# Kernel optimization log

Measured on AMD Instinct MI355X. Metric: run time of the kernel, lower is better.

Reference implementation:

```python
import jax, jax.numpy as jnp
import numpy as np


def setup_inputs() -> dict:
    key = jax.random.key(0)
    kq, kk, kv = jax.random.split(key, 3)
    B, H, N, D = 2, 16, 2048, 64
    q = jax.random.normal(kq, (B, H, N, D), dtype=jnp.float32)
    k = jax.random.normal(kk, (B, H, N, D), dtype=jnp.float32)
    v = jax.random.normal(kv, (B, H, N, D), dtype=jnp.float32)
    return {"q": q, "k": k, "v": v}


def reference(q, k, v):
    # RBF-kernel causal attention: logits = -relu(||q-k||^2) / sqrt(D)
    B, H, N, D = q.shape
    sm_scale = 1.0 / jnp.sqrt(jnp.asarray(D, dtype=q.dtype))
    q_sq = jnp.sum(q * q, axis=-1)              # [B,H,N]
    k_sq = jnp.sum(k * k, axis=-1)              # [B,H,N]
    qk = jnp.einsum("bhmd,bhnd->bhmn", q, k)    # [B,H,N,N]
    dist_sq = q_sq[..., :, None] + k_sq[..., None, :] - 2.0 * qk
    dist_sq = jnp.maximum(dist_sq, 0.0)         # relu on squared distance
    logits = -dist_sq * sm_scale
    # causal mask: query m attends to keys n <= m
    causal = jnp.tril(jnp.ones((N, N), dtype=bool))
    logits = jnp.where(causal, logits, -jnp.inf)
    p = jax.nn.softmax(logits, axis=-1)
    out = jnp.einsum("bhmn,bhnd->bhmd", p, v)
    return out
```

## Files before the change

### kernel.cpp

```cpp
#include <hip/hip_runtime.h>

#define NN 2048
#define DD 64
#define C1 0.36067376f
#define C1H 0.18033688f

typedef _Float16 h8 __attribute__((ext_vector_type(8)));
typedef _Float16 h4 __attribute__((ext_vector_type(4)));
typedef float f32x16 __attribute__((ext_vector_type(16)));

union H8U4 { h8 v; unsigned u[4]; };

__global__ __launch_bounds__(64) void prep(const float* __restrict__ k,
                                           const float* __restrict__ v,
                                           _Float16* __restrict__ Ks,
                                           _Float16* __restrict__ Vs,
                                           float* __restrict__ hk) {
    __shared__ _Float16 T[32][72];
    const int jj = blockIdx.x, bh = blockIdx.y, lane = threadIdx.x;
    const int ln = lane & 31, lh = lane >> 5;
    const size_t ibase = (size_t)bh * NN * DD + (size_t)jj * 32 * DD;

    {
        const float* kr = k + ibase + (size_t)ln * DD;
        float s = 0.f;
#pragma unroll
        for (int c = 0; c < 4; ++c) {
            float4 a = *(const float4*)&kr[16 * c + 8 * lh];
            float4 b = *(const float4*)&kr[16 * c + 8 * lh + 4];
            h8 o = {(_Float16)a.x, (_Float16)a.y, (_Float16)a.z, (_Float16)a.w,
                    (_Float16)b.x, (_Float16)b.y, (_Float16)b.z, (_Float16)b.w};
            *(h8*)&Ks[((size_t)bh * 16384 + jj * 256 + c * 64 + lh * 32 + ln) * 8] = o;
            s += a.x*a.x + a.y*a.y + a.z*a.z + a.w*a.w
               + b.x*b.x + b.y*b.y + b.z*b.z + b.w*b.w;
        }
        s += __shfl_xor(s, 32);
        if (lh == 0) hk[bh * NN + jj * 32 + ln] = s * C1H;
    }

#pragma unroll
    for (int t = 0; t < 8; ++t) {
        int f = lane + 64 * t;
        int row = f >> 4, c4 = (f & 15) * 4;
        float4 a = *(const float4*)&v[ibase + (size_t)row * DD + c4];
        h4 hv = {(_Float16)a.x, (_Float16)a.y, (_Float16)a.z, (_Float16)a.w};
        *(h4*)&T[row][c4] = hv;
    }
    __syncthreads();
#pragma unroll
    for (int oc = 0; oc < 4; ++oc) {
        int o = oc >> 1, c = oc & 1;
        h8 r;
#pragma unroll
        for (int jx = 0; jx < 8; ++jx) r[jx] = T[16 * c + 8 * lh + jx][32 * o + ln];
        *(h8*)&Vs[((size_t)bh * 16384 + jj * 256 + o * 128 + c * 64 + lh * 32 + ln) * 8] = r;
    }
}

__global__ __launch_bounds__(128, 2) void rbf_attn(
    const float* __restrict__ q, const _Float16* __restrict__ Ks,
    const _Float16* __restrict__ Vs, const float* __restrict__ hk,
    float* __restrict__ out)
{
    const int tid = threadIdx.x;
    const int bh = blockIdx.x;
    const int qb = 31 - blockIdx.y;
    const int wv = tid >> 6, lane = tid & 63;
    const int ln = lane & 31, lh = lane >> 5;
    const int jmax = 2 * qb + wv;
    const int qrow = qb * 64 + wv * 32 + ln;
    const size_t fbase = (size_t)bh * NN * DD;

    h8 qf[4];
    {
        const float* qr = q + fbase + (size_t)qrow * DD;
#pragma unroll
        for (int c = 0; c < 4; ++c) {
            float4 a = *(const float4*)&qr[16 * c + 8 * lh];
            float4 b = *(const float4*)&qr[16 * c + 8 * lh + 4];
            qf[c] = h8{(_Float16)a.x, (_Float16)a.y, (_Float16)a.z, (_Float16)a.w,
                       (_Float16)b.x, (_Float16)b.y, (_Float16)b.z, (_Float16)b.w};
        }
    }

    const _Float16* Ksb = Ks + (size_t)bh * 131072;
    const _Float16* Vsb = Vs + (size_t)bh * 131072;
    const float4* hk4 = (const float4*)(hk + bh * NN);
    const int klq = (lh * 32 + ln) * 8;

    f32x16 O0, O1;
#pragma unroll
    for (int r = 0; r < 16; ++r) { O0[r] = 0.f; O1[r] = 0.f; }
    float lsum = 0.f, mrun = -INFINITY;

    auto loadT = [&](int jj, h8 (&kf)[4], h8 (&vf)[4], float4 (&hr)[4]) {
        const _Float16* kp = Ksb + (size_t)jj * 2048 + klq;
        const _Float16* vp = Vsb + (size_t)jj * 2048 + klq;
#pragma unroll
        for (int c = 0; c < 4; ++c) kf[c] = *(const h8*)(kp + c * 512);
#pragma unroll
        for (int oc = 0; oc < 4; ++oc)
            vf[oc] = *(const h8*)(vp + (oc >> 1) * 1024 + (oc & 1) * 512);
#pragma unroll
        for (int g = 0; g < 4; ++g) hr[g] = hk4[jj * 8 + g * 2 + lh];
    };

    auto comp = [&](int jj, h8 (&kf)[4], h8 (&vf)[4], float4 (&hr)[4]) {
        f32x16 S;
#pragma unroll
        for (int r = 0; r < 16; ++r) S[r] = 0.f;
#pragma unroll
        for (int c = 0; c < 4; ++c)
            S = __builtin_amdgcn_mfma_f32_32x32x16_f16(kf[c], qf[c], S, 0, 0, 0);

        const bool diag = (jj == jmax);
        float x[16];
#pragma unroll
        for (int r = 0; r < 16; ++r) {
            const float* hf = (const float*)&hr[r >> 2];
            float xv = fmaf(S[r], C1, -hf[r & 3]);
            if (diag) {
                int keyloc = (r & 3) + 8 * (r >> 2) + 4 * lh;
                if (keyloc > ln) xv = -INFINITY;
            }
            x[r] = xv;
        }
        float mt = x[0];
#pragma unroll
        for (int r = 1; r < 16; ++r) mt = fmaxf(mt, x[r]);
        mt = fmaxf(mt, __shfl_xor(mt, 32));
        float mnew = fmaxf(mrun, mt);
        float alpha = __builtin_amdgcn_exp2f(mrun - mnew);
        mrun = mnew;
        float p[16], ps = 0.f;
#pragma unroll
        for (int r = 0; r < 16; ++r) {
            p[r] = __builtin_amdgcn_exp2f(x[r] - mnew);
            ps += p[r];
        }
        lsum = fmaf(lsum, alpha, ps);
#pragma unroll
        for (int r = 0; r < 16; ++r) { O0[r] *= alpha; O1[r] *= alpha; }

        unsigned pk[8];
#pragma unroll
        for (int hh = 0; hh < 8; ++hh) {
            auto pr = __builtin_amdgcn_cvt_pkrtz(p[2 * hh], p[2 * hh + 1]);
            unsigned pu; __builtin_memcpy(&pu, &pr, 4);
            pk[hh] = pu;
        }
#pragma unroll
        for (int s = 0; s < 2; ++s) {
            unsigned send0 = lh ? pk[4 * s + 0] : pk[4 * s + 2];
            unsigned send1 = lh ? pk[4 * s + 1] : pk[4 * s + 3];
            unsigned r0 = (unsigned)__shfl_xor((int)send0, 32);
            unsigned r1 = (unsigned)__shfl_xor((int)send1, 32);
            H8U4 pb;
            pb.u[0] = lh ? r0 : pk[4 * s + 0];
            pb.u[1] = lh ? r1 : pk[4 * s + 1];
            pb.u[2] = lh ? pk[4 * s + 2] : r0;
            pb.u[3] = lh ? pk[4 * s + 3] : r1;
            O0 = __builtin_amdgcn_mfma_f32_32x32x16_f16(vf[s], pb.v, O0, 0, 0, 0);
            O1 = __builtin_amdgcn_mfma_f32_32x32x16_f16(vf[2 + s], pb.v, O1, 0, 0, 0);
        }
    };

    h8 kfA[4], vfA[4]; float4 hrA[4];
    h8 kfB[4], vfB[4]; float4 hrB[4];
    loadT(0, kfA, vfA, hrA);
    int jj = 0;
    while (true) {
        if (jj < jmax) loadT(jj + 1, kfB, vfB, hrB);
        comp(jj, kfA, vfA, hrA);
        if (++jj > jmax) break;
        if (jj < jmax) loadT(jj + 1, kfA, vfA, hrA);
        comp(jj, kfB, vfB, hrB);
        if (++jj > jmax) break;
    }

    float lt = lsum + __shfl_xor(lsum, 32);
    float inv = 1.f / lt;
    size_t ro = fbase + (size_t)qrow * DD;
#pragma unroll
    for (int g = 0; g < 4; ++g) {
        float4 o0 = make_float4(O0[4 * g + 0] * inv, O0[4 * g + 1] * inv,
                                O0[4 * g + 2] * inv, O0[4 * g + 3] * inv);
        *(float4*)&out[ro + 8 * g + 4 * lh] = o0;
        float4 o1 = make_float4(O1[4 * g + 0] * inv, O1[4 * g + 1] * inv,
                                O1[4 * g + 2] * inv, O1[4 * g + 3] * inv);
        *(float4*)&out[ro + 32 + 8 * g + 4 * lh] = o1;
    }
}

extern "C" void kernel_launch(void* const* d_in, const int* in_sizes, int n_in,
                              void* d_out, int out_size, void* d_ws, size_t ws_size,
                              hipStream_t stream) {
    (void)in_sizes; (void)n_in; (void)out_size; (void)ws_size;
    const float* q = (const float*)d_in[0];
    const float* k = (const float*)d_in[1];
    const float* v = (const float*)d_in[2];
    float* out = (float*)d_out;

    float* hk = (float*)d_ws;
    _Float16* Ks = (_Float16*)((char*)d_ws + 262144);
    _Float16* Vs = (_Float16*)((char*)d_ws + 262144 + 8388608);

    prep<<<dim3(64, 32), 64, 0, stream>>>(k, v, Ks, Vs, hk);
    rbf_attn<<<dim3(32, 32), 128, 0, stream>>>(q, Ks, Vs, hk, out);
}
```

Before: 137.9 us.

## Split key range across two waves per 32-row query tile with LDS merge

Measured after the change: 130.4 us. 5.4% less time.

```diff
diff --git a/kernel.cpp b/kernel.cpp
--- a/kernel.cpp
+++ b/kernel.cpp
@@ -62,13 +62,13 @@
     const _Float16* __restrict__ Vs, const float* __restrict__ hk,
     float* __restrict__ out)
 {
+    __shared__ float sm[64][34];
     const int tid = threadIdx.x;
     const int bh = blockIdx.x;
-    const int qb = 31 - blockIdx.y;
+    const int qt = 63 - (int)blockIdx.y;
     const int wv = tid >> 6, lane = tid & 63;
     const int ln = lane & 31, lh = lane >> 5;
-    const int jmax = 2 * qb + wv;
-    const int qrow = qb * 64 + wv * 32 + ln;
+    const int qrow = qt * 32 + ln;
     const size_t fbase = (size_t)bh * NN * DD;
 
     h8 qf[4];
@@ -93,6 +93,11 @@
     for (int r = 0; r < 16; ++r) { O0[r] = 0.f; O1[r] = 0.f; }
     float lsum = 0.f, mrun = -INFINITY;
 
+    const int T = qt + 1;
+    const int half = (T + 1) >> 1;
+    const int j0 = wv ? half : 0;
+    const int j1 = wv ? T : half;
+
     auto loadT = [&](int jj, h8 (&kf)[4], h8 (&vf)[4], float4 (&hr)[4]) {
         const _Float16* kp = Ksb + (size_t)jj * 2048 + klq;
         const _Float16* vp = Vsb + (size_t)jj * 2048 + klq;
@@ -113,7 +118,7 @@
         for (int c = 0; c < 4; ++c)
             S = __builtin_amdgcn_mfma_f32_32x32x16_f16(kf[c], qf[c], S, 0, 0, 0);
 
-        const bool diag = (jj == jmax);
+        const bool diag = (jj == qt);
         float x[16];
 #pragma unroll
         for (int r = 0; r < 16; ++r) {
@@ -167,28 +172,50 @@
 
     h8 kfA[4], vfA[4]; float4 hrA[4];
     h8 kfB[4], vfB[4]; float4 hrB[4];
-    loadT(0, kfA, vfA, hrA);
-    int jj = 0;
-    while (true) {
-        if (jj < jmax) loadT(jj + 1, kfB, vfB, hrB);
-        comp(jj, kfA, vfA, hrA);
-        if (++jj > jmax) break;
-        if (jj < jmax) loadT(jj + 1, kfA, vfA, hrA);
-        comp(jj, kfB, vfB, hrB);
-        if (++jj > jmax) break;
-    }
-
-    float lt = lsum + __shfl_xor(lsum, 32);
-    float inv = 1.f / lt;
-    size_t ro = fbase + (size_t)qrow * DD;
-#pragma unroll
-    for (int g = 0; g < 4; ++g) {
-        float4 o0 = make_float4(O0[4 * g + 0] * inv, O0[4 * g + 1] * inv,
-                                O0[4 * g + 2] * inv, O0[4 * g + 3] * inv);
-        *(float4*)&out[ro + 8 * g + 4 * lh] = o0;
-        float4 o1 = make_float4(O1[4 * g + 0] * inv, O1[4 * g + 1] * inv,
-                                O1[4 * g + 2] * inv, O1[4 * g + 3] * inv);
-        *(float4*)&out[ro + 32 + 8 * g + 4 * lh] = o1;
+    if (j0 < j1) {
+        loadT(j0, kfA, vfA, hrA);
+        int jj = j0;
+        while (true) {
+            if (jj + 1 < j1) loadT(jj + 1, kfB, vfB, hrB);
+            comp(jj, kfA, vfA, hrA);
+            if (++jj >= j1) break;
+            if (jj + 1 < j1) loadT(jj + 1, kfA, vfA, hrA);
+            comp(jj, kfB, vfB, hrB);
+            if (++jj >= j1) break;
+        }
+    }
+
+    if (wv) {
+#pragma unroll
+        for (int r = 0; r < 16; ++r) { sm[lane][r] = O0[r]; sm[lane][16 + r] = O1[r]; }
+        sm[lane][32] = lsum + __shfl_xor(lsum, 32);
+        sm[lane][33] = mrun;
+    }
+    __syncthreads();
+    if (!wv) {
+        float l0 = lsum + __shfl_xor(lsum, 32);
+        float l1 = sm[lane][32];
+        float m1 = sm[lane][33];
+        float m = fmaxf(mrun, m1);
+        float a0 = __builtin_amdgcn_exp2f(mrun - m);
+        float a1 = __builtin_amdgcn_exp2f(m1 - m);
+        float lt = l0 * a0 + l1 * a1;
+        float inv = 1.f / lt;
+        float s0 = a0 * inv, s1 = a1 * inv;
+        size_t ro = fbase + (size_t)qrow * DD;
+#pragma unroll
+        for (int g = 0; g < 4; ++g) {
+            float4 o0 = make_float4(O0[4 * g + 0] * s0 + sm[lane][4 * g + 0] * s1,
+                                    O0[4 * g + 1] * s0 + sm[lane][4 * g + 1] * s1,
+                                    O0[4 * g + 2] * s0 + sm[lane][4 * g + 2] * s1,
+                                    O0[4 * g + 3] * s0 + sm[lane][4 * g + 3] * s1);
+            *(float4*)&out[ro + 8 * g + 4 * lh] = o0;
+            float4 o1 = make_float4(O1[4 * g + 0] * s0 + sm[lane][16 + 4 * g + 0] * s1,
+                                    O1[4 * g + 1] * s0 + sm[lane][16 + 4 * g + 1] * s1,
+                                    O1[4 * g + 2] * s0 + sm[lane][16 + 4 * g + 2] * s1,
+                                    O1[4 * g + 3] * s0 + sm[lane][16 + 4 * g + 3] * s1);
+            *(float4*)&out[ro + 32 + 8 * g + 4 * lh] = o1;
+        }
     }
 }
 
@@ -206,5 +233,5 @@
     _Float16* Vs = (_Float16*)((char*)d_ws + 262144 + 8388608);
 
     prep<<<dim3(64, 32), 64, 0, stream>>>(k, v, Ks, Vs, hk);
-    rbf_attn<<<dim3(32, 32), 128, 0, stream>>>(q, Ks, Vs, hk, out);
+    rbf_attn<<<dim3(32, 64), 128, 0, stream>>>(q, Ks, Vs, hk, out);
 }
```

## Pair light and heavy causal query tiles per block with split-K waves

Applied to the files above, without the earlier changes.

Result: faster. 129.6 us (-6.0%).

```diff
diff --git a/kernel.cpp b/kernel.cpp
--- a/kernel.cpp
+++ b/kernel.cpp
@@ -62,24 +62,29 @@
     const _Float16* __restrict__ Vs, const float* __restrict__ hk,
     float* __restrict__ out)
 {
+    __shared__ float sm[2][64][34];
     const int tid = threadIdx.x;
     const int bh = blockIdx.x;
-    const int qb = 31 - blockIdx.y;
+    const int pr = blockIdx.y;
+    const int qt1 = pr, qt2 = 63 - pr;
     const int wv = tid >> 6, lane = tid & 63;
     const int ln = lane & 31, lh = lane >> 5;
-    const int jmax = 2 * qb + wv;
-    const int qrow = qb * 64 + wv * 32 + ln;
     const size_t fbase = (size_t)bh * NN * DD;
 
-    h8 qf[4];
+    h8 qf1[4], qf2[4];
     {
-        const float* qr = q + fbase + (size_t)qrow * DD;
+        const float* qr1 = q + fbase + (size_t)(qt1 * 32 + ln) * DD;
+        const float* qr2 = q + fbase + (size_t)(qt2 * 32 + ln) * DD;
 #pragma unroll
         for (int c = 0; c < 4; ++c) {
-            float4 a = *(const float4*)&qr[16 * c + 8 * lh];
-            float4 b = *(const float4*)&qr[16 * c + 8 * lh + 4];
-            qf[c] = h8{(_Float16)a.x, (_Float16)a.y, (_Float16)a.z, (_Float16)a.w,
-                       (_Float16)b.x, (_Float16)b.y, (_Float16)b.z, (_Float16)b.w};
+            float4 a = *(const float4*)&qr1[16 * c + 8 * lh];
+            float4 b = *(const float4*)&qr1[16 * c + 8 * lh + 4];
+            qf1[c] = h8{(_Float16)a.x, (_Float16)a.y, (_Float16)a.z, (_Float16)a.w,
+                        (_Float16)b.x, (_Float16)b.y, (_Float16)b.z, (_Float16)b.w};
+            float4 e = *(const float4*)&qr2[16 * c + 8 * lh];
+            float4 f = *(const float4*)&qr2[16 * c + 8 * lh + 4];
+            qf2[c] = h8{(_Float16)e.x, (_Float16)e.y, (_Float16)e.z, (_Float16)e.w,
+                        (_Float16)f.x, (_Float16)f.y, (_Float16)f.z, (_Float16)f.w};
         }
     }
 
@@ -88,24 +93,26 @@
     const float4* hk4 = (const float4*)(hk + bh * NN);
     const int klq = (lh * 32 + ln) * 8;
 
-    f32x16 O0, O1;
-#pragma unroll
-    for (int r = 0; r < 16; ++r) { O0[r] = 0.f; O1[r] = 0.f; }
-    float lsum = 0.f, mrun = -INFINITY;
-
-    auto loadT = [&](int jj, h8 (&kf)[4], h8 (&vf)[4], float4 (&hr)[4]) {
+    f32x16 O0a, O1a, O0b, O1b;
+#pragma unroll
+    for (int r = 0; r < 16; ++r) { O0a[r] = 0.f; O1a[r] = 0.f; O0b[r] = 0.f; O1b[r] = 0.f; }
+    float l1 = 0.f, m1 = -INFINITY;
+    float l2 = 0.f, m2 = -INFINITY;
+
+    const int T1 = qt1 + 1, T2 = qt2 + 1;
+    const int h2 = (T2 + 1) >> 1;
+    const int j0 = wv ? h2 : 0;
+    const int j1 = wv ? T2 : h2;
+
+    auto loadK = [&](int jj, h8 (&kf)[4]) {
         const _Float16* kp = Ksb + (size_t)jj * 2048 + klq;
-        const _Float16* vp = Vsb + (size_t)jj * 2048 + klq;
 #pragma unroll
         for (int c = 0; c < 4; ++c) kf[c] = *(const h8*)(kp + c * 512);
-#pragma unroll
-        for (int oc = 0; oc < 4; ++oc)
-            vf[oc] = *(const h8*)(vp + (oc >> 1) * 1024 + (oc & 1) * 512);
-#pragma unroll
-        for (int g = 0; g < 4; ++g) hr[g] = hk4[jj * 8 + g * 2 + lh];
     };
 
-    auto comp = [&](int jj, h8 (&kf)[4], h8 (&vf)[4], float4 (&hr)[4]) {
+    auto compQ = [&](int jj, const h8 (&kf)[4], const h8 (&vf)[4],
+                     const float4 (&hr)[4], const h8 (&qf)[4],
+                     f32x16& O0, f32x16& O1, float& mrun, float& lsum, int dqt) {
         f32x16 S;
 #pragma unroll
         for (int r = 0; r < 16; ++r) S[r] = 0.f;
@@ -113,7 +120,7 @@
         for (int c = 0; c < 4; ++c)
             S = __builtin_amdgcn_mfma_f32_32x32x16_f16(kf[c], qf[c], S, 0, 0, 0);
 
-        const bool diag = (jj == jmax);
+        const bool diag = (jj == dqt);
         float x[16];
 #pragma unroll
         for (int r = 0; r < 16; ++r) {
@@ -125,19 +132,21 @@
             }
             x[r] = xv;
         }
-        float mt = x[0];
-#pragma unroll
-        for (int r = 1; r < 16; ++r) mt = fmaxf(mt, x[r]);
+        float a0 = fmaxf(x[0], x[1]),  a1 = fmaxf(x[2], x[3]);
+        float a2 = fmaxf(x[4], x[5]),  a3 = fmaxf(x[6], x[7]);
+        float a4 = fmaxf(x[8], x[9]),  a5 = fmaxf(x[10], x[11]);
+        float a6 = fmaxf(x[12], x[13]), a7 = fmaxf(x[14], x[15]);
+        float mt = fmaxf(fmaxf(fmaxf(a0, a1), fmaxf(a2, a3)),
+                         fmaxf(fmaxf(a4, a5), fmaxf(a6, a7)));
         mt = fmaxf(mt, __shfl_xor(mt, 32));
         float mnew = fmaxf(mrun, mt);
         float alpha = __builtin_amdgcn_exp2f(mrun - mnew);
         mrun = mnew;
-        float p[16], ps = 0.f;
-#pragma unroll
-        for (int r = 0; r < 16; ++r) {
-            p[r] = __builtin_amdgcn_exp2f(x[r] - mnew);
-            ps += p[r];
-        }
+        float p[16], ps;
+#pragma unroll
+        for (int r = 0; r < 16; ++r) p[r] = __builtin_amdgcn_exp2f(x[r] - mnew);
+        ps = (((p[0] + p[1]) + (p[2] + p[3])) + ((p[4] + p[5]) + (p[6] + p[7])))
+           + (((p[8] + p[9]) + (p[10] + p[11])) + ((p[12] + p[13]) + (p[14] + p[15])));
         lsum = fmaf(lsum, alpha, ps);
 #pragma unroll
         for (int r = 0; r < 16; ++r) { O0[r] *= alpha; O1[r] *= alpha; }
@@ -145,8 +154,8 @@
         unsigned pk[8];
 #pragma unroll
         for (int hh = 0; hh < 8; ++hh) {
-            auto pr = __builtin_amdgcn_cvt_pkrtz(p[2 * hh], p[2 * hh + 1]);
-            unsigned pu; __builtin_memcpy(&pu, &pr, 4);
+            auto prr = __builtin_amdgcn_cvt_pkrtz(p[2 * hh], p[2 * hh + 1]);
+            unsigned pu; __builtin_memcpy(&pu, &prr, 4);
             pk[hh] = pu;
         }
 #pragma unroll
@@ -165,30 +174,75 @@
         }
     };
 
-    h8 kfA[4], vfA[4]; float4 hrA[4];
-    h8 kfB[4], vfB[4]; float4 hrB[4];
-    loadT(0, kfA, vfA, hrA);
-    int jj = 0;
+    auto compPair = [&](int jj, const h8 (&kf)[4]) {
+        float4 hr[4];
+#pragma unroll
+        for (int g = 0; g < 4; ++g) hr[g] = hk4[jj * 8 + g * 2 + lh];
+        h8 vf[4];
+        const _Float16* vp = Vsb + (size_t)jj * 2048 + klq;
+#pragma unroll
+        for (int oc = 0; oc < 4; ++oc)
+            vf[oc] = *(const h8*)(vp + (oc >> 1) * 1024 + (oc & 1) * 512);
+        compQ(jj, kf, vf, hr, qf2, O0b, O1b, m2, l2, qt2);
+        if (jj < T1)
+            compQ(jj, kf, vf, hr, qf1, O0a, O1a, m1, l1, qt1);
+    };
+
+    h8 kfA[4], kfB[4];
+    loadK(j0, kfA);
+    int jj = j0;
     while (true) {
-        if (jj < jmax) loadT(jj + 1, kfB, vfB, hrB);
-        comp(jj, kfA, vfA, hrA);
-        if (++jj > jmax) break;
-        if (jj < jmax) loadT(jj + 1, kfA, vfA, hrA);
-        comp(jj, kfB, vfB, hrB);
-        if (++jj > jmax) break;
-    }
-
-    float lt = lsum + __shfl_xor(lsum, 32);
-    float inv = 1.f / lt;
-    size_t ro = fbase + (size_t)qrow * DD;
-#pragma unroll
-    for (int g = 0; g < 4; ++g) {
-        float4 o0 = make_float4(O0[4 * g + 0] * inv, O0[4 * g + 1] * inv,
-                                O0[4 * g + 2] * inv, O0[4 * g + 3] * inv);
-        *(float4*)&out[ro + 8 * g + 4 * lh] = o0;
-        float4 o1 = make_float4(O1[4 * g + 0] * inv, O1[4 * g + 1] * inv,
-                                O1[4 * g + 2] * inv, O1[4 * g + 3] * inv);
-        *(float4*)&out[ro + 32 + 8 * g + 4 * lh] = o1;
+        if (jj + 1 < j1) loadK(jj + 1, kfB);
+        compPair(jj, kfA);
+        if (++jj >= j1) break;
+        if (jj + 1 < j1) loadK(jj + 1, kfA);
+        compPair(jj, kfB);
+        if (++jj >= j1) break;
+    }
+
+    if (wv) {
+#pragma unroll
+        for (int r = 0; r < 16; ++r) {
+            sm[0][lane][r] = O0a[r]; sm[0][lane][16 + r] = O1a[r];
+            sm[1][lane][r] = O0b[r]; sm[1][lane][16 + r] = O1b[r];
+        }
+        sm[0][lane][32] = l1 + __shfl_xor(l1, 32);
+        sm[0][lane][33] = m1;
+        sm[1][lane][32] = l2 + __shfl_xor(l2, 32);
+        sm[1][lane][33] = m2;
+    }
+    __syncthreads();
+    if (!wv) {
+        auto mergeStore = [&](int si, const f32x16& O0, const f32x16& O1,
+                              float mrun, float lsum, int qt) {
+            float l0 = lsum + __shfl_xor(lsum, 32);
+            float lo = sm[si][lane][32];
+            float mo = sm[si][lane][33];
+            float m = fmaxf(mrun, mo);
+            float a0 = __builtin_amdgcn_exp2f(mrun - m);
+            float a1 = __builtin_amdgcn_exp2f(mo - m);
+            float lt = l0 * a0 + lo * a1;
+            float inv = 1.f / lt;
+            float s0 = a0 * inv, s1 = a1 * inv;
+            size_t ro = fbase + (size_t)(qt * 32 + ln) * DD;
+#pragma unroll
+            for (int g = 0; g < 4; ++g) {
+                float4 o0 = make_float4(
+                    O0[4 * g + 0] * s0 + sm[si][lane][4 * g + 0] * s1,
+                    O0[4 * g + 1] * s0 + sm[si][lane][4 * g + 1] * s1,
+                    O0[4 * g + 2] * s0 + sm[si][lane][4 * g + 2] * s1,
+                    O0[4 * g + 3] * s0 + sm[si][lane][4 * g + 3] * s1);
+                *(float4*)&out[ro + 8 * g + 4 * lh] = o0;
+                float4 o1 = make_float4(
+                    O1[4 * g + 0] * s0 + sm[si][lane][16 + 4 * g + 0] * s1,
+                    O1[4 * g + 1] * s0 + sm[si][lane][16 + 4 * g + 1] * s1,
+                    O1[4 * g + 2] * s0 + sm[si][lane][16 + 4 * g + 2] * s1,
+                    O1[4 * g + 3] * s0 + sm[si][lane][16 + 4 * g + 3] * s1);
+                *(float4*)&out[ro + 32 + 8 * g + 4 * lh] = o1;
+            }
+        };
+        mergeStore(0, O0a, O1a, m1, l1, qt1);
+        mergeStore(1, O0b, O1b, m2, l2, qt2);
     }
 }
 
```
